# Optimization experiments

Hardware: AMD Instinct MI355X
Metric: run time of the kernel (lower is better)

Reference implementation:

```python
import jax, jax.numpy as jnp
import numpy as np

N_HEAD = 16
ROPE_THETA = 10000.0


def setup_inputs() -> dict:
    key = jax.random.key(0)
    k0, k1, k2 = jax.random.split(key, 3)
    B, T, C = 2, 2048, 1024
    s = 0.02  # GPT-2 style init scale
    return {
        "x": jax.random.normal(k0, (B, T, C), jnp.float32),
        "w_attn": jax.random.normal(k1, (C, 3 * C), jnp.float32) * s,
        "b_attn": jnp.zeros((3 * C,), jnp.float32),
        "w_proj": jax.random.normal(k2, (C, C), jnp.float32) * s,
        "b_proj": jnp.zeros((C,), jnp.float32),
    }


def _rope(x):
    # x: [B, H, T, D]; interleaved-pair rotary (lucidrains rotate_queries_or_keys)
    T, D = x.shape[-2], x.shape[-1]
    inv_freq = 1.0 / (ROPE_THETA ** (jnp.arange(0, D, 2, dtype=jnp.float32) / D))
    freqs = jnp.arange(T, dtype=jnp.float32)[:, None] * inv_freq[None, :]  # [T, D/2]
    emb = jnp.repeat(freqs, 2, axis=-1)  # [T, D], each freq duplicated per pair
    cos, sin = jnp.cos(emb), jnp.sin(emb)
    xr = x.reshape(*x.shape[:-1], D // 2, 2)
    x1, x2 = xr[..., 0], xr[..., 1]
    rot = jnp.stack((-x2, x1), axis=-1).reshape(x.shape)  # rotate_half
    return x * cos + rot * sin


def reference(x, w_attn, b_attn, w_proj, b_proj):
    B, T, C = x.shape
    H = N_HEAD
    D = C // H
    qkv = x @ w_attn + b_attn                      # [B, T, 3C]
    q, k, v = jnp.split(qkv, 3, axis=-1)

    def heads(t):
        return t.reshape(B, T, H, D).transpose(0, 2, 1, 3)  # [B, H, T, D]

    q, k, v = heads(q), heads(k), heads(v)
    q = _rope(q)
    k = _rope(k)

    att = jnp.einsum("bhqd,bhkd->bhqk", q, k) * (1.0 / np.sqrt(D))
    causal = jnp.tril(jnp.ones((T, T), dtype=bool))
    att = jnp.where(causal, att, -jnp.inf)
    att = jax.nn.softmax(att, axis=-1)
    y = jnp.einsum("bhqk,bhkd->bhqd", att, v)
    y = y.transpose(0, 2, 1, 3).reshape(B, T, C)
    return y @ w_proj + b_proj
```

## Files before the change

kernel.cpp:

```cpp
#include <hip/hip_runtime.h>
#include <hip/hip_bf16.h>
#include <stdint.h>

typedef __hip_bfloat16 bf16;
typedef __attribute__((ext_vector_type(8))) short bf16x8;
typedef __attribute__((ext_vector_type(4))) float f32x4;

__device__ inline float bf2f(bf16 v) { return __bfloat162float(v); }
__device__ inline bf16 f2bf(float f) { return __float2bfloat16(f); }

__device__ inline void glds16(const void* g, void* l) {
    __builtin_amdgcn_global_load_lds(
        (const __attribute__((address_space(1))) uint32_t*)g,
        (__attribute__((address_space(3))) uint32_t*)l, 16, 0, 0);
}

__global__ __launch_bounds__(256) void conv_x(const float* __restrict__ in,
                                              bf16* __restrict__ out)
{
    size_t i = ((size_t)blockIdx.x * 256 + threadIdx.x) * 8;
    float4 f0 = *(const float4*)(in + i);
    float4 f1 = *(const float4*)(in + i + 4);
    union { bf16x8 v; bf16 e[8]; } u;
    u.e[0] = f2bf(f0.x); u.e[1] = f2bf(f0.y); u.e[2] = f2bf(f0.z); u.e[3] = f2bf(f0.w);
    u.e[4] = f2bf(f1.x); u.e[5] = f2bf(f1.y); u.e[6] = f2bf(f1.z); u.e[7] = f2bf(f1.w);
    *(bf16x8*)(out + i) = u.v;
}

__global__ __launch_bounds__(256) void conv_wt(const float* __restrict__ W,
                                               bf16* __restrict__ Wt, int N, int K)
{
    __shared__ bf16 t[64][72];
    const int n0 = blockIdx.x * 64, k0 = blockIdx.y * 64;
    const int tid = threadIdx.x;
#pragma unroll
    for (int p = 0; p < 4; ++p) {
        int idx = p * 256 + tid;
        int kr = idx >> 4, c4 = idx & 15;
        float4 f = *(const float4*)(W + (size_t)(k0 + kr) * N + n0 + c4 * 4);
        t[kr][c4 * 4 + 0] = f2bf(f.x); t[kr][c4 * 4 + 1] = f2bf(f.y);
        t[kr][c4 * 4 + 2] = f2bf(f.z); t[kr][c4 * 4 + 3] = f2bf(f.w);
    }
    __syncthreads();
#pragma unroll
    for (int p = 0; p < 2; ++p) {
        int idx = p * 256 + tid;
        int nr = idx >> 3, ch = idx & 7;
        union { bf16x8 v; bf16 e[8]; } u;
#pragma unroll
        for (int j = 0; j < 8; ++j) u.e[j] = t[ch * 8 + j][nr];
        *(bf16x8*)(Wt + (size_t)(n0 + nr) * K + k0 + ch * 8) = u.v;
    }
}

template <bool OUTF32>
__global__ __launch_bounds__(256) void gemm_bt(
    const bf16* __restrict__ A, const bf16* __restrict__ Bt,
    const float* __restrict__ bias, int M, int N, int K, void* __restrict__ outv)
{
    __shared__ __align__(16) bf16 sa[128 * 32];
    __shared__ __align__(16) bf16 sb[128 * 32];

    const int tid  = threadIdx.x;
    const int wave = tid >> 6, lane = tid & 63;
    const int quad = lane >> 4, l16 = lane & 15;
    const int wm = wave >> 1, wn = wave & 1;
    const int row0 = blockIdx.x * 128, n0 = blockIdx.y * 128;

    f32x4 acc[4][4] = {};

    const int sm = wave * 16 + (lane >> 2);
    const int sk = (lane & 3) * 8;
    const bf16* ga = A  + (size_t)(row0 + sm) * K + sk;
    const bf16* gb = Bt + (size_t)(n0  + sm) * K + sk;
    bf16* la = sa + wave * 512;
    bf16* lb = sb + wave * 512;

    for (int k0 = 0; k0 < K; k0 += 32) {
        __syncthreads();
        glds16(ga + k0, la);
        glds16(ga + k0 + (size_t)64 * K, la + 2048);
        glds16(gb + k0, lb);
        glds16(gb + k0 + (size_t)64 * K, lb + 2048);
        __syncthreads();

        bf16x8 af[4], bfr[4];
#pragma unroll
        for (int mi = 0; mi < 4; ++mi)
            af[mi] = *(const bf16x8*)&sa[(wm * 64 + mi * 16 + l16) * 32 + quad * 8];
#pragma unroll
        for (int ni = 0; ni < 4; ++ni)
            bfr[ni] = *(const bf16x8*)&sb[(wn * 64 + ni * 16 + l16) * 32 + quad * 8];
#pragma unroll
        for (int mi = 0; mi < 4; ++mi)
#pragma unroll
            for (int ni = 0; ni < 4; ++ni)
                acc[mi][ni] = __builtin_amdgcn_mfma_f32_16x16x32_bf16(
                    af[mi], bfr[ni], acc[mi][ni], 0, 0, 0);
    }

#pragma unroll
    for (int ni = 0; ni < 4; ++ni) {
        int col = n0 + wn * 64 + ni * 16 + l16;
        float bvv = bias[col];
#pragma unroll
        for (int mi = 0; mi < 4; ++mi) {
#pragma unroll
            for (int r = 0; r < 4; ++r) {
                int row = row0 + wm * 64 + mi * 16 + quad * 4 + r;
                float v = acc[mi][ni][r] + bvv;
                if (OUTF32) ((float*)outv)[(size_t)row * N + col] = v;
                else        ((bf16*)outv)[(size_t)row * N + col] = f2bf(v);
            }
        }
    }
}

__global__ __launch_bounds__(256) void rope_k(
    const bf16* __restrict__ qkv, bf16* __restrict__ q, bf16* __restrict__ k)
{
    int gid = blockIdx.x * 256 + threadIdx.x;
    int p  = gid & 31, d0 = p * 2;
    int t  = (gid >> 5) & 2047;
    int h  = (gid >> 16) & 15;
    int b  = gid >> 20;

    size_t src = ((size_t)(b * 2048 + t)) * 3072 + h * 64 + d0;
    size_t dst = (((size_t)(b * 16 + h)) * 2048 + t) * 64 + d0;

    float invf = expf(-(float)d0 * (9.210340371976184f / 64.0f));
    float sn, cs;
    sincosf((float)t * invf, &sn, &cs);

    const float QS = 0.125f * 1.44269504088896f;
    float q0 = bf2f(qkv[src]),        q1 = bf2f(qkv[src + 1]);
    float k0 = bf2f(qkv[src + 1024]), k1 = bf2f(qkv[src + 1025]);
    q[dst]     = f2bf((q0 * cs - q1 * sn) * QS);
    q[dst + 1] = f2bf((q1 * cs + q0 * sn) * QS);
    k[dst]     = f2bf(k0 * cs - k1 * sn);
    k[dst + 1] = f2bf(k1 * cs + k0 * sn);
}

__global__ __launch_bounds__(256) void transpose_v(
    const bf16* __restrict__ qkv, bf16* __restrict__ vt)
{
    __shared__ bf16 t[64][72];
    const int t0 = blockIdx.x * 64;
    const int bh = blockIdx.y, b = bh >> 4, h = bh & 15;
    const int tid = threadIdx.x;
#pragma unroll
    for (int p = 0; p < 2; ++p) {
        int idx = p * 256 + tid;
        int tr = idx >> 3, ch = idx & 7;
        bf16x8 v = *(const bf16x8*)(qkv + ((size_t)(b * 2048 + t0 + tr)) * 3072
                                    + 2048 + h * 64 + ch * 8);
#pragma unroll
        for (int j = 0; j < 8; ++j) t[tr][ch * 8 + j] = ((const bf16*)&v)[j];
    }
    __syncthreads();
#pragma unroll
    for (int p = 0; p < 2; ++p) {
        int idx = p * 256 + tid;
        int dr = idx >> 3, ch = idx & 7;
        union { bf16x8 v; bf16 e[8]; } u;
#pragma unroll
        for (int j = 0; j < 8; ++j) u.e[j] = t[ch * 8 + j][dr];
        *(bf16x8*)(vt + ((size_t)bh * 64 + dr) * 2048 + t0 + ch * 8) = u.v;
    }
}

__global__ __launch_bounds__(256) void attn_k(
    const bf16* __restrict__ qg, const bf16* __restrict__ kg,
    const bf16* __restrict__ vtg, bf16* __restrict__ y)
{
    __shared__ __align__(16) bf16 sK[64 * 64];
    __shared__ __align__(16) bf16 sV[64 * 64];
    __shared__ __align__(16) bf16 pL[4][16][72];

    const int tid  = threadIdx.x;
    const int wave = tid >> 6, lane = tid & 63;
    const int quad = lane >> 4, l16 = lane & 15;
    const int bh   = blockIdx.x;
    const int qt   = 31 - (int)blockIdx.y;
    const bf16* Q  = qg  + (size_t)bh * 2048 * 64;
    const bf16* K  = kg  + (size_t)bh * 2048 * 64;
    const bf16* Vt = vtg + (size_t)bh * 64 * 2048;
    const int b = bh >> 4, h = bh & 15;

    const int q0 = qt * 64 + wave * 16;

    bf16x8 aq[2];
    aq[0] = *(const bf16x8*)(Q + (size_t)(q0 + l16) * 64 + quad * 8);
    aq[1] = *(const bf16x8*)(Q + (size_t)(q0 + l16) * 64 + 32 + quad * 8);

    f32x4 o[4] = {};
    float m_r[4] = {-1e30f, -1e30f, -1e30f, -1e30f};
    float l_r[4] = {0.f, 0.f, 0.f, 0.f};

    for (int kt = 0; kt <= q0 + 15; kt += 64) {
        __syncthreads();
#pragma unroll
        for (int c = 0; c < 2; ++c) {
            int key = wave * 16 + c * 8 + (lane >> 3);
            int p   = lane & 7;
            glds16(K + (size_t)(kt + key) * 64 + ((p ^ key) & 7) * 8,
                   &sK[(wave * 16 + c * 8) * 64]);
        }
#pragma unroll
        for (int c = 0; c < 2; ++c) {
            int d = wave * 16 + c * 8 + (lane >> 3);
            int p = lane & 7;
            glds16(Vt + (size_t)d * 2048 + kt + ((p ^ d) & 7) * 8,
                   &sV[(wave * 16 + c * 8) * 64]);
        }
        __syncthreads();

        const int nlast = min(3, (q0 - kt) >> 4);
        f32x4 sc[4];
        __builtin_amdgcn_s_setprio(1);
#pragma unroll
        for (int nt = 0; nt < 4; ++nt) {
            if (nt > nlast) continue;
            int key = nt * 16 + l16;
            f32x4 s0 = {};
            bf16x8 bk0 = *(const bf16x8*)&sK[key * 64 + ((quad ^ key) & 7) * 8];
            s0 = __builtin_amdgcn_mfma_f32_16x16x32_bf16(aq[0], bk0, s0, 0, 0, 0);
            bf16x8 bk1 = *(const bf16x8*)&sK[key * 64 + (((4 + quad) ^ key) & 7) * 8];
            sc[nt] = __builtin_amdgcn_mfma_f32_16x16x32_bf16(aq[1], bk1, s0, 0, 0, 0);
        }
        __builtin_amdgcn_s_setprio(0);
        {
            const int diag = (q0 - kt) >> 4;
            if (diag <= 3) {
                int key = kt + diag * 16 + l16;
#pragma unroll
                for (int r = 0; r < 4; ++r) {
                    int row = q0 + quad * 4 + r;
                    if (key > row) sc[diag][r] = -1e30f;
                }
            }
        }
        float rowmax[4] = {-1e30f, -1e30f, -1e30f, -1e30f};
#pragma unroll
        for (int nt = 0; nt < 4; ++nt) {
            if (nt > nlast) continue;
#pragma unroll
            for (int r = 0; r < 4; ++r) rowmax[r] = fmaxf(rowmax[r], sc[nt][r]);
        }
#pragma unroll
        for (int off = 1; off < 16; off <<= 1)
#pragma unroll
            for (int r = 0; r < 4; ++r)
                rowmax[r] = fmaxf(rowmax[r], __shfl_xor(rowmax[r], off));

        float alpha[4];
#pragma unroll
        for (int r = 0; r < 4; ++r) {
            float mn = fmaxf(m_r[r], rowmax[r]);
            alpha[r] = exp2f(m_r[r] - mn);
            m_r[r] = mn;
        }
        float rs[4] = {0.f, 0.f, 0.f, 0.f};
#pragma unroll
        for (int nt = 0; nt < 4; ++nt) {
            if (nt > nlast) continue;
#pragma unroll
            for (int r = 0; r < 4; ++r) {
                float p = exp2f(sc[nt][r] - m_r[r]);
                sc[nt][r] = p;
                rs[r] += p;
            }
        }
#pragma unroll
        for (int off = 1; off < 16; off <<= 1)
#pragma unroll
            for (int r = 0; r < 4; ++r) rs[r] += __shfl_xor(rs[r], off);
#pragma unroll
        for (int r = 0; r < 4; ++r) l_r[r] = l_r[r] * alpha[r] + rs[r];
#pragma unroll
        for (int nt = 0; nt < 4; ++nt)
#pragma unroll
            for (int r = 0; r < 4; ++r) o[nt][r] *= alpha[r];

#pragma unroll
        for (int nt = 0; nt < 4; ++nt) {
            if (nt > nlast) continue;
            int blk = (2 * nt + (l16 >> 3)) ^ quad;
#pragma unroll
            for (int r = 0; r < 4; ++r)
                pL[wave][quad * 4 + r][blk * 8 + (l16 & 7)] = f2bf(sc[nt][r]);
        }
        if (nlast < 3 && !(nlast & 1)) {
            int blk = (2 * (nlast + 1) + (l16 >> 3)) ^ quad;
#pragma unroll
            for (int r = 0; r < 4; ++r)
                pL[wave][quad * 4 + r][blk * 8 + (l16 & 7)] = f2bf(0.f);
        }
        __builtin_amdgcn_s_setprio(1);
#pragma unroll
        for (int c = 0; c < 2; ++c) {
            if (c > (nlast >> 1)) continue;
            bf16x8 pa = *(const bf16x8*)&pL[wave][l16][(((4 * c + quad) ^ (l16 >> 2)) * 8)];
#pragma unroll
            for (int dnt = 0; dnt < 4; ++dnt) {
                int d = dnt * 16 + l16;
                int cc = c * 4 + quad;
                bf16x8 vb = *(const bf16x8*)&sV[d * 64 + ((cc ^ d) & 7) * 8];
                o[dnt] = __builtin_amdgcn_mfma_f32_16x16x32_bf16(pa, vb, o[dnt], 0, 0, 0);
            }
        }
        __builtin_amdgcn_s_setprio(0);
    }

#pragma unroll
    for (int r = 0; r < 4; ++r) {
        float inv = 1.0f / l_r[r];
        int qq = q0 + quad * 4 + r;
#pragma unroll
        for (int nt = 0; nt < 4; ++nt) {
            int d = nt * 16 + l16;
            y[((size_t)(b * 2048 + qq)) * 1024 + h * 64 + d] = f2bf(o[nt][r] * inv);
        }
    }
}

extern "C" void kernel_launch(void* const* d_in, const int* in_sizes, int n_in,
                              void* d_out, int out_size, void* d_ws, size_t ws_size,
                              hipStream_t stream) {
    const float* x      = (const float*)d_in[0];
    const float* w_attn = (const float*)d_in[1];
    const float* b_attn = (const float*)d_in[2];
    const float* w_proj = (const float*)d_in[3];
    const float* b_proj = (const float*)d_in[4];
    float* out = (float*)d_out;

    bf16* xbf = (bf16*)d_ws;
    bf16* wat = xbf + (size_t)4194304;
    bf16* wpt = wat + (size_t)3145728;
    bf16* qkv = wpt + (size_t)1048576;
    bf16* qh  = qkv + (size_t)12582912;
    bf16* kh  = qh  + (size_t)4194304;
    bf16* vt  = kh  + (size_t)4194304;
    bf16* yws = vt  + (size_t)4194304;

    dim3 blk(256);
    conv_x<<<dim3(2048), blk, 0, stream>>>(x, xbf);
    conv_wt<<<dim3(48, 16), blk, 0, stream>>>(w_attn, wat, 3072, 1024);
    conv_wt<<<dim3(16, 16), blk, 0, stream>>>(w_proj, wpt, 1024, 1024);
    gemm_bt<false><<<dim3(32, 24), blk, 0, stream>>>(xbf, wat, b_attn,
                                                     4096, 3072, 1024, qkv);
    rope_k<<<dim3(8192), blk, 0, stream>>>(qkv, qh, kh);
    transpose_v<<<dim3(32, 32), blk, 0, stream>>>(qkv, vt);
    attn_k<<<dim3(32, 32), blk, 0, stream>>>(qh, kh, vt, yws);
    gemm_bt<true><<<dim3(32, 8), blk, 0, stream>>>(yws, wpt, b_proj,
                                                   4096, 1024, 1024, out);
    (void)in_sizes; (void)n_in; (void)ws_size; (void)out_size;
}
```

Before: 240.7 us.

## Double-buffer K/V tiles in attention and compute row sums via MFMA

The attention kernel now keeps two shared-memory buffers for K and V and issues the async global-to-LDS load of the next key tile before computing on the current one, with one barrier per iteration instead of two. This is meant to hide global load latency behind the QK and PV matrix work. Separately, the softmax row sum is no longer built from per-lane adds and a shuffle reduction; it is taken from an extra MFMA of the bf16 probabilities against a vector of ones. That sum now uses the bf16-rounded probabilities, which matches what feeds the PV product, and it doubles K/V LDS usage, which may lower occupancy.

```diff
diff --git a/kernel.cpp b/kernel.cpp
--- a/kernel.cpp
+++ b/kernel.cpp
@@ -173,8 +173,8 @@
     const bf16* __restrict__ qg, const bf16* __restrict__ kg,
     const bf16* __restrict__ vtg, bf16* __restrict__ y)
 {
-    __shared__ __align__(16) bf16 sK[64 * 64];
-    __shared__ __align__(16) bf16 sV[64 * 64];
+    __shared__ __align__(16) bf16 sK[2][64 * 64];
+    __shared__ __align__(16) bf16 sV[2][64 * 64];
     __shared__ __align__(16) bf16 pL[4][16][72];
 
     const int tid  = threadIdx.x;
@@ -193,27 +193,40 @@
     aq[0] = *(const bf16x8*)(Q + (size_t)(q0 + l16) * 64 + quad * 8);
     aq[1] = *(const bf16x8*)(Q + (size_t)(q0 + l16) * 64 + 32 + quad * 8);
 
+    union { bf16x8 v; short e[8]; } uo;
+#pragma unroll
+    for (int j = 0; j < 8; ++j) uo.e[j] = (short)0x3F80;
+    const bf16x8 vones = uo.v;
+
     f32x4 o[4] = {};
+    f32x4 ls   = {};
     float m_r[4] = {-1e30f, -1e30f, -1e30f, -1e30f};
-    float l_r[4] = {0.f, 0.f, 0.f, 0.f};
-
-    for (int kt = 0; kt <= q0 + 15; kt += 64) {
-        __syncthreads();
+
+    auto stage = [&](int bsel, int kt) {
 #pragma unroll
         for (int c = 0; c < 2; ++c) {
             int key = wave * 16 + c * 8 + (lane >> 3);
             int p   = lane & 7;
             glds16(K + (size_t)(kt + key) * 64 + ((p ^ key) & 7) * 8,
-                   &sK[(wave * 16 + c * 8) * 64]);
+                   &sK[bsel][(wave * 16 + c * 8) * 64]);
         }
 #pragma unroll
         for (int c = 0; c < 2; ++c) {
             int d = wave * 16 + c * 8 + (lane >> 3);
             int p = lane & 7;
             glds16(Vt + (size_t)d * 2048 + kt + ((p ^ d) & 7) * 8,
-                   &sV[(wave * 16 + c * 8) * 64]);
-        }
-        __syncthreads();
+                   &sV[bsel][(wave * 16 + c * 8) * 64]);
+        }
+    };
+
+    const int niter = qt + 1;
+    stage(0, 0);
+    __syncthreads();
+
+    int cur = 0;
+    for (int it = 0; it < niter; ++it) {
+        const int kt = it * 64;
+        if (it + 1 < niter) stage(cur ^ 1, kt + 64);
 
         const int nlast = min(3, (q0 - kt) >> 4);
         f32x4 sc[4];
@@ -223,9 +236,9 @@
             if (nt > nlast) continue;
             int key = nt * 16 + l16;
             f32x4 s0 = {};
-            bf16x8 bk0 = *(const bf16x8*)&sK[key * 64 + ((quad ^ key) & 7) * 8];
+            bf16x8 bk0 = *(const bf16x8*)&sK[cur][key * 64 + ((quad ^ key) & 7) * 8];
             s0 = __builtin_amdgcn_mfma_f32_16x16x32_bf16(aq[0], bk0, s0, 0, 0, 0);
-            bf16x8 bk1 = *(const bf16x8*)&sK[key * 64 + (((4 + quad) ^ key) & 7) * 8];
+            bf16x8 bk1 = *(const bf16x8*)&sK[cur][key * 64 + (((4 + quad) ^ key) & 7) * 8];
             sc[nt] = __builtin_amdgcn_mfma_f32_16x16x32_bf16(aq[1], bk1, s0, 0, 0, 0);
         }
         __builtin_amdgcn_s_setprio(0);
@@ -260,27 +273,18 @@
             alpha[r] = exp2f(m_r[r] - mn);
             m_r[r] = mn;
         }
-        float rs[4] = {0.f, 0.f, 0.f, 0.f};
 #pragma unroll
         for (int nt = 0; nt < 4; ++nt) {
             if (nt > nlast) continue;
 #pragma unroll
-            for (int r = 0; r < 4; ++r) {
-                float p = exp2f(sc[nt][r] - m_r[r]);
-                sc[nt][r] = p;
-                rs[r] += p;
-            }
-        }
-#pragma unroll
-        for (int off = 1; off < 16; off <<= 1)
-#pragma unroll
-            for (int r = 0; r < 4; ++r) rs[r] += __shfl_xor(rs[r], off);
-#pragma unroll
-        for (int r = 0; r < 4; ++r) l_r[r] = l_r[r] * alpha[r] + rs[r];
+            for (int r = 0; r < 4; ++r) sc[nt][r] = exp2f(sc[nt][r] - m_r[r]);
+        }
 #pragma unroll
         for (int nt = 0; nt < 4; ++nt)
 #pragma unroll
             for (int r = 0; r < 4; ++r) o[nt][r] *= alpha[r];
+#pragma unroll
+        for (int r = 0; r < 4; ++r) ls[r] *= alpha[r];
 
 #pragma unroll
         for (int nt = 0; nt < 4; ++nt) {
@@ -301,20 +305,24 @@
         for (int c = 0; c < 2; ++c) {
             if (c > (nlast >> 1)) continue;
             bf16x8 pa = *(const bf16x8*)&pL[wave][l16][(((4 * c + quad) ^ (l16 >> 2)) * 8)];
+            ls = __builtin_amdgcn_mfma_f32_16x16x32_bf16(pa, vones, ls, 0, 0, 0);
 #pragma unroll
             for (int dnt = 0; dnt < 4; ++dnt) {
                 int d = dnt * 16 + l16;
                 int cc = c * 4 + quad;
-                bf16x8 vb = *(const bf16x8*)&sV[d * 64 + ((cc ^ d) & 7) * 8];
+                bf16x8 vb = *(const bf16x8*)&sV[cur][d * 64 + ((cc ^ d) & 7) * 8];
                 o[dnt] = __builtin_amdgcn_mfma_f32_16x16x32_bf16(pa, vb, o[dnt], 0, 0, 0);
             }
         }
         __builtin_amdgcn_s_setprio(0);
+
+        __syncthreads();
+        cur ^= 1;
     }
 
 #pragma unroll
     for (int r = 0; r < 4; ++r) {
-        float inv = 1.0f / l_r[r];
+        float inv = 1.0f / ls[r];
         int qq = q0 + quad * 4 + r;
 #pragma unroll
         for (int nt = 0; nt < 4; ++nt) {
```

Measured after the change: 237.6 us. No clear change (-1.3%).
